# Kernel tuning notes

Measured on AMD Instinct MI355X. Metric: run time of the kernel, lower is better.

Reference implementation:

```python
import jax, jax.numpy as jnp
import numpy as np

B, DIM, HEADS, HH, WW = 4, 256, 8, 48, 48
N = HH * WW
CS = DIM // 4  # channels per crpe split / lowpass split = 64
POOL_SIZES = (1, 2, 3, 6)


def _constrain(kern, k):
    # kern: (C, C, k*k-1); insert the constrained -1 center tap, reshape to OIHW
    C = kern.shape[0]
    ctr = (k * k) // 2
    full = jnp.concatenate(
        [kern[:, :, :ctr], -jnp.ones((C, C, 1), kern.dtype), kern[:, :, ctr:]], axis=2)
    return full.reshape(C, C, k, k)


def _conv(x, w, k):
    p = k // 2
    return jax.lax.conv_general_dilated(
        x, w, (1, 1), [(p, p), (p, p)],
        dimension_numbers=('NCHW', 'OIHW', 'NCHW'))


def _upsample_bilinear_ac(x, H, W):
    # bilinear, align_corners=True, from (B,C,sh,sw) to (B,C,H,W)
    Bc, Cc, sh, sw = x.shape
    if sh == 1 and sw == 1:
        return jnp.broadcast_to(x, (Bc, Cc, H, W))
    ys = jnp.arange(H, dtype=x.dtype) * ((sh - 1) / (H - 1))
    xs = jnp.arange(W, dtype=x.dtype) * ((sw - 1) / (W - 1))
    y0 = jnp.floor(ys).astype(jnp.int32)
    x0 = jnp.floor(xs).astype(jnp.int32)
    y1 = jnp.minimum(y0 + 1, sh - 1)
    x1 = jnp.minimum(x0 + 1, sw - 1)
    wy = (ys - y0.astype(x.dtype))[:, None]
    wx = (xs - x0.astype(x.dtype))[None, :]
    v00 = x[:, :, y0[:, None], x0[None, :]]
    v01 = x[:, :, y0[:, None], x1[None, :]]
    v10 = x[:, :, y1[:, None], x0[None, :]]
    v11 = x[:, :, y1[:, None], x1[None, :]]
    return (v00 * (1 - wy) * (1 - wx) + v01 * (1 - wy) * wx
            + v10 * wy * (1 - wx) + v11 * wy * wx)


def _lowpass(v):
    # v: (B,C,H,W); H,W divisible by all pool sizes -> adaptive pool == uniform block mean
    Bc, Cc, Hc, Wc = v.shape
    outs = []
    for c, s in zip(jnp.split(v, 4, axis=1), POOL_SIZES):
        p = c.reshape(Bc, Cc // 4, s, Hc // s, s, Wc // s).mean(axis=(3, 5))
        outs.append(_upsample_bilinear_ac(p, Hc, Wc))
    return jax.nn.relu(jnp.concatenate(outs, axis=1))


def _crpe(q, res, Hc, Wc, kern3, kern5, kern7):
    # q: (B,h,N,Ch); res: (B,N,C)
    Bc, h, Nc, Ch = q.shape
    C = h * Ch
    v = res.transpose(0, 2, 1).reshape(Bc, C, Hc, Wc)
    lp = _lowpass(v)
    v0, v1, v2, v3 = jnp.split(v, 4, axis=1)
    conv_v = jnp.concatenate([
        v0,
        _conv(v1, _constrain(kern3, 3), 3),
        _conv(v2, _constrain(kern5, 5), 5),
        _conv(v3, _constrain(kern7, 7), 7)], axis=1)
    conv_v = conv_v.reshape(Bc, h, Ch, Nc).transpose(0, 1, 3, 2)  # B h N Ch
    lp = lp.reshape(Bc, h, Ch, Nc).transpose(0, 1, 3, 2)
    return q * conv_v + lp


def setup_inputs() -> dict:
    key = jax.random.key(0)
    ks = jax.random.split(key, 9)
    x = jax.random.normal(ks[0], (B, N, DIM), jnp.float32)
    wq = jax.random.normal(ks[1], (DIM, DIM), jnp.float32) * 0.02
    wkv = jax.random.normal(ks[2], (2 * DIM, DIM), jnp.float32) * 0.02
    wres = jax.random.normal(ks[3], (DIM, DIM), jnp.float32) * 0.02
    wproj = jax.random.normal(ks[4], (DIM, DIM), jnp.float32) * 0.02
    bproj = jnp.zeros((DIM,), jnp.float32)
    def base_kernel(k, kk):
        kern = jax.random.uniform(k, (CS, CS, kk * kk - 1), jnp.float32)
        return kern / kern.sum(axis=2, keepdims=True)
    kern3 = base_kernel(ks[5], 3)
    kern5 = base_kernel(ks[6], 5)
    kern7 = base_kernel(ks[7], 7)
    return {'x': x, 'H': HH, 'W': WW, 'wq': wq, 'wkv': wkv, 'wres': wres,
            'wproj': wproj, 'bproj': bproj, 'kern3': kern3, 'kern5': kern5,
            'kern7': kern7}


def reference(x, H, W, wq, wkv, wres, wproj, bproj, kern3, kern5, kern7):
    Bc, Nc, C = x.shape
    h = HEADS
    Ch = C // h
    scale = Ch ** -0.5
    q = (x @ wq.T).reshape(Bc, Nc, h, Ch).transpose(0, 2, 1, 3)          # B h N Ch
    kv = (x @ wkv.T).reshape(Bc, Nc, 2, h, Ch).transpose(2, 0, 3, 1, 4)  # 2 B h N Ch
    k, v = kv[0], kv[1]
    attn = jax.nn.softmax(jnp.einsum('bhnc,bhmc->bhnm', q * scale, k), axis=-1)
    res = jax.nn.relu(x @ wres.T)
    crpe = _crpe(q, res, H, W, kern3, kern5, kern7)
    out = (jnp.einsum('bhnm,bhmc->bhnc', attn, v) + crpe)
    out = out.transpose(0, 2, 1, 3).reshape(Bc, Nc, C)
    return out @ wproj.T + bproj
```

## Files before the change

### kernel.cpp

```cpp
#include <hip/hip_runtime.h>
#include <math.h>

#define NTOK 2304
#define DIMC 256

typedef __attribute__((ext_vector_type(8))) short short8;
typedef __attribute__((ext_vector_type(4))) float f32x4;

__device__ __forceinline__ unsigned short f2bf(float f) {
  unsigned u = __float_as_uint(f);
  u += 0x7fffu + ((u >> 16) & 1u);
  return (unsigned short)(u >> 16);
}
__device__ __forceinline__ float bf2f(unsigned short h) {
  return __uint_as_float(((unsigned)h) << 16);
}
__device__ __forceinline__ unsigned pack2(float a, float b) {
  return (unsigned)f2bf(a) | ((unsigned)f2bf(b) << 16);
}
__device__ __forceinline__ float fexp2(float x) {
#if __has_builtin(__builtin_amdgcn_exp2f)
  return __builtin_amdgcn_exp2f(x);
#else
  return exp2f(x);
#endif
}
__device__ __forceinline__ void split4(float4 v, uint2& hp, uint2& lp) {
  unsigned short h0 = f2bf(v.x), h1 = f2bf(v.y), h2 = f2bf(v.z), h3 = f2bf(v.w);
  unsigned short l0 = f2bf(v.x - bf2f(h0)), l1 = f2bf(v.y - bf2f(h1));
  unsigned short l2 = f2bf(v.z - bf2f(h2)), l3 = f2bf(v.w - bf2f(h3));
  hp.x = (unsigned)h0 | ((unsigned)h1 << 16);
  hp.y = (unsigned)h2 | ((unsigned)h3 << 16);
  lp.x = (unsigned)l0 | ((unsigned)l1 << 16);
  lp.y = (unsigned)l2 | ((unsigned)l3 << 16);
}

__global__ __launch_bounds__(256) void k_prep_all(
    const float* __restrict__ x, const float* __restrict__ wq,
    const float* __restrict__ wkv, const float* __restrict__ wres,
    const float* __restrict__ wproj, const float* __restrict__ k3,
    const float* __restrict__ k5, const float* __restrict__ k7,
    unsigned short* __restrict__ xhi, unsigned short* __restrict__ xlo,
    unsigned short* __restrict__ Whi, unsigned short* __restrict__ Wlo,
    unsigned short* __restrict__ pwhi, unsigned short* __restrict__ pwlo,
    unsigned short* __restrict__ wT) {
  int bx = blockIdx.x;
  int tid = threadIdx.x;
  if (bx < 2304) {
    int i = bx * 256 + tid;
    uint2 hp, lp;
    split4(((const float4*)x)[i], hp, lp);
    ((uint2*)xhi)[i] = hp;
    ((uint2*)xlo)[i] = lp;
  } else if (bx < 2560) {
    int idx = (bx - 2304) * 256 + tid;
    int row = idx >> 6, q4 = idx & 63;
    const float* src;
    if (row < 256)      src = wq + (size_t)row * 256;
    else if (row < 768) src = wkv + (size_t)(row - 256) * 256;
    else                src = wres + (size_t)(row - 768) * 256;
    uint2 hp, lp;
    split4(*(const float4*)(src + q4 * 4), hp, lp);
    ((uint2*)Whi)[idx] = hp;
    ((uint2*)Wlo)[idx] = lp;
  } else if (bx < 2624) {
    int idx = (bx - 2560) * 256 + tid;
    uint2 hp, lp;
    split4(((const float4*)wproj)[idx], hp, lp);
    ((uint2*)pwhi)[idx] = hp;
    ((uint2*)pwlo)[idx] = lp;
  } else {
    int idx = (bx - 2624) * 256 + tid;
    const float* src; int K, tloc;
    if (idx < 9 * 4096)       { K = 3; src = k3; tloc = idx >> 12; }
    else if (idx < 34 * 4096) { K = 5; src = k5; tloc = (idx - 9 * 4096) >> 12; }
    else                      { K = 7; src = k7; tloc = (idx - 34 * 4096) >> 12; }
    int r = idx & 4095, oc = r >> 6, ic = r & 63;
    int K2 = K * K, ctr = K2 / 2;
    float v = (tloc == ctr) ? -1.f
            : src[((size_t)oc * 64 + ic) * (K2 - 1) + (tloc < ctr ? tloc : tloc - 1)];
    wT[idx] = f2bf(v);
  }
}

__global__ __launch_bounds__(512, 2) void k_gemm_qkvres_mfma(
    const unsigned short* __restrict__ xhi, const unsigned short* __restrict__ xlo,
    const unsigned short* __restrict__ Whi, const unsigned short* __restrict__ Wlo,
    float* __restrict__ qb, unsigned short* __restrict__ khi,
    unsigned short* __restrict__ klo, unsigned short* __restrict__ vT,
    float* __restrict__ resb, unsigned short* __restrict__ resT) {
  __shared__ __align__(16) unsigned short Ah[128 * 64];
  __shared__ __align__(16) unsigned short Al[128 * 64];
  __shared__ __align__(16) unsigned short Bh[128 * 64];
  __shared__ __align__(16) unsigned short Bl[128 * 64];
  const int tid = threadIdx.x;
  const int row0 = blockIdx.x * 128;
  const int col0 = blockIdx.y * 128;
  const int w = tid >> 6, lane = tid & 63, lg = lane >> 4, lc = lane & 15;
  const int wm = w >> 1, wn = w & 1;

  f32x4 acc[2][4];
#pragma unroll
  for (int i = 0; i < 2; ++i)
#pragma unroll
    for (int j = 0; j < 4; ++j) acc[i][j] = (f32x4){0.f, 0.f, 0.f, 0.f};

  for (int kc = 0; kc < 256; kc += 64) {
    __syncthreads();
#pragma unroll
    for (int l = 0; l < 2; ++l) {
      int idx = tid + l * 512;
      int r = idx >> 3, o = idx & 7;
      int sl = ((o ^ (r & 7))) * 8;
      *(uint4*)&Ah[r * 64 + sl] = *(const uint4*)&xhi[(size_t)(row0 + r) * 256 + kc + o * 8];
      *(uint4*)&Al[r * 64 + sl] = *(const uint4*)&xlo[(size_t)(row0 + r) * 256 + kc + o * 8];
      *(uint4*)&Bh[r * 64 + sl] = *(const uint4*)&Whi[(size_t)(col0 + r) * 256 + kc + o * 8];
      *(uint4*)&Bl[r * 64 + sl] = *(const uint4*)&Wlo[(size_t)(col0 + r) * 256 + kc + o * 8];
    }
    __syncthreads();
#pragma unroll
    for (int ks = 0; ks < 2; ++ks) {
      short8 ah[2], al[2], bh[4], bl[4];
#pragma unroll
      for (int mi = 0; mi < 2; ++mi) {
        int r = wm * 32 + mi * 16 + lc;
        int sl = (((ks * 4 + lg) ^ (r & 7))) * 8;
        ah[mi] = *(short8*)&Ah[r * 64 + sl];
        al[mi] = *(short8*)&Al[r * 64 + sl];
      }
#pragma unroll
      for (int ni = 0; ni < 4; ++ni) {
        int r = wn * 64 + ni * 16 + lc;
        int sl = (((ks * 4 + lg) ^ (r & 7))) * 8;
        bh[ni] = *(short8*)&Bh[r * 64 + sl];
        bl[ni] = *(short8*)&Bl[r * 64 + sl];
      }
#pragma unroll
      for (int mi = 0; mi < 2; ++mi)
#pragma unroll
        for (int ni = 0; ni < 4; ++ni) {
          acc[mi][ni] = __builtin_amdgcn_mfma_f32_16x16x32_bf16(ah[mi], bh[ni], acc[mi][ni], 0, 0, 0);
          acc[mi][ni] = __builtin_amdgcn_mfma_f32_16x16x32_bf16(ah[mi], bl[ni], acc[mi][ni], 0, 0, 0);
          acc[mi][ni] = __builtin_amdgcn_mfma_f32_16x16x32_bf16(al[mi], bh[ni], acc[mi][ni], 0, 0, 0);
        }
    }
  }

#pragma unroll
  for (int mi = 0; mi < 2; ++mi) {
    int rbase = row0 + wm * 32 + mi * 16 + lg * 4;
#pragma unroll
    for (int ni = 0; ni < 4; ++ni) {
      int col = col0 + wn * 64 + ni * 16 + lc;
#pragma unroll
      for (int j = 0; j < 4; ++j) {
        int row = rbase + j;
        int b = row / NTOK, n = row % NTOK;
        float vv = acc[mi][ni][j];
        if (col < 256) {
          int head = col >> 5, ch = col & 31;
          qb[(((size_t)b * 8 + head) * NTOK + n) * 32 + ch] = vv;
        } else if (col < 512) {
          int o = col - 256; int head = o >> 5, ch = o & 31;
          size_t idx = (((size_t)b * 8 + head) * NTOK + n) * 32 + ch;
          unsigned short h = f2bf(vv);
          khi[idx] = h;
          klo[idx] = f2bf(vv - bf2f(h));
        } else if (col < 768) {
          int o = col - 512; int head = o >> 5, ch = o & 31;
          vT[(((size_t)b * 8 + head) * 32 + ch) * NTOK + n] = f2bf(vv);
        } else {
          int c = col - 768;
          float rv = fmaxf(vv, 0.f);
          resb[((size_t)b * 256 + c) * NTOK + n] = rv;
          if (c >= 64) {
            int g = (c >> 6) - 1, ic = c & 63;
            resT[(((size_t)b * 3 + g) * NTOK + n) * 64 + ic] = f2bf(rv);
          }
        }
      }
    }
  }
}

__device__ __forceinline__ void softmax_pv(
    f32x4 (&s)[8], float& m_r, float& l_r, f32x4& o0, f32x4& o1,
    int lg, int lc, int srcA, unsigned short (*vs)[136]) {
  float mx[8];
#pragma unroll
  for (int nt = 0; nt < 8; ++nt)
    mx[nt] = fmaxf(fmaxf(s[nt][0], s[nt][1]), fmaxf(s[nt][2], s[nt][3]));
  float mloc = fmaxf(fmaxf(fmaxf(mx[0], mx[1]), fmaxf(mx[2], mx[3])),
                     fmaxf(fmaxf(mx[4], mx[5]), fmaxf(mx[6], mx[7])));

  if (__any(mloc > m_r + 8.f)) {
    float mt = mloc;
    mt = fmaxf(mt, __shfl_xor(mt, 16, 64));
    mt = fmaxf(mt, __shfl_xor(mt, 32, 64));
    float mn = fmaxf(m_r, mt);
    float corr = fexp2(m_r - mn);
    m_r = mn;
    l_r *= corr;
#pragma unroll
    for (int j = 0; j < 4; ++j) {
      float cj = __shfl(corr, lg * 4 + j, 64);
      o0[j] *= cj;
      o1[j] *= cj;
    }
  }

  float ls = 0.f;
#pragma unroll
  for (int nt = 0; nt < 8; ++nt)
#pragma unroll
    for (int j = 0; j < 4; ++j) {
      float p = fexp2(s[nt][j] - m_r);
      s[nt][j] = p;
      ls += p;
    }
  l_r += ls;

  unsigned W[8][2];
#pragma unroll
  for (int nt = 0; nt < 8; ++nt) {
    W[nt][0] = pack2(s[nt][0], s[nt][1]);
    W[nt][1] = pack2(s[nt][2], s[nt][3]);
  }

  __builtin_amdgcn_s_setprio(1);
#pragma unroll
  for (int h2 = 0; h2 < 4; ++h2) {
    unsigned v0 = (lg & 2) ? W[2 * h2 + 1][0] : W[2 * h2][0];
    unsigned v1 = (lg & 2) ? W[2 * h2 + 1][1] : W[2 * h2][1];
    union { unsigned u[4]; short8 v; } pa;
    pa.u[0] = (unsigned)__shfl((int)v0, srcA, 64);
    pa.u[1] = (unsigned)__shfl((int)v1, srcA, 64);
    pa.u[2] = (unsigned)__shfl((int)v0, srcA + 16, 64);
    pa.u[3] = (unsigned)__shfl((int)v1, srcA + 16, 64);
    short8 vf0 = *(short8*)&vs[lc][h2 * 32 + lg * 8];
    short8 vf1 = *(short8*)&vs[lc + 16][h2 * 32 + lg * 8];
    o0 = __builtin_amdgcn_mfma_f32_16x16x32_bf16(pa.v, vf0, o0, 0, 0, 0);
    o1 = __builtin_amdgcn_mfma_f32_16x16x32_bf16(pa.v, vf1, o1, 0, 0, 0);
  }
  __builtin_amdgcn_s_setprio(0);
}

__device__ __forceinline__ void attn_body(
    int bh, int qt, int tid,
    const float* __restrict__ qb, const unsigned short* __restrict__ khi,
    const unsigned short* __restrict__ klo, const unsigned short* __restrict__ vT,
    float* __restrict__ accb,
    unsigned short (*ks_hi)[40], unsigned short (*vs)[136]) {
  const int r0 = qt * 64;
  const int w = tid >> 6;
  const int lane = tid & 63;
  const int lg = lane >> 4;
  const int lc = lane & 15;

  const float scale = 0.17677669529663688f * 1.4426950408889634f;

  const float* qp = qb + (((size_t)bh * NTOK + r0 + w * 16 + lc) * 32 + lg * 8);
  float qf[8];
  *(float4*)&qf[0] = *(const float4*)qp;
  *(float4*)&qf[4] = *(const float4*)(qp + 4);
  short8 qh, ql;
#pragma unroll
  for (int i = 0; i < 8; ++i) {
    float v = qf[i] * scale;
    unsigned short h = f2bf(v);
    qh[i] = (short)h;
    ql[i] = (short)f2bf(v - bf2f(h));
  }

  float m_r = -1.0e30f;
  float l_r = 0.f;
  f32x4 o0 = {0.f, 0.f, 0.f, 0.f};
  f32x4 o1 = {0.f, 0.f, 0.f, 0.f};

  const int krow = tid >> 1, kseg = (tid & 1) * 16;
  const int vrow = tid >> 3, vseg = (tid & 7) * 16;

  const unsigned short* khs = khi + ((size_t)bh * NTOK + krow) * 32 + kseg;
  const unsigned short* vsrc = vT + ((size_t)bh * 32 + vrow) * NTOK + vseg;
  const unsigned short* klp = klo + ((size_t)bh * NTOK + lc) * 32 + lg * 8;

  uint4 ph0 = *(const uint4*)khs,  ph1 = *(const uint4*)(khs + 8);
  uint4 pv0 = *(const uint4*)vsrc, pv1 = *(const uint4*)(vsrc + 8);

  const int srcA = ((lg & 1) * 2) * 16 + lc;

  for (int kt = 0; kt < 18; ++kt) {
    const int kv0 = kt * 128;
    __syncthreads();
    *(uint4*)&ks_hi[krow][kseg]     = ph0;
    *(uint4*)&ks_hi[krow][kseg + 8] = ph1;
    *(uint4*)&vs[vrow][vseg]        = pv0;
    *(uint4*)&vs[vrow][vseg + 8]    = pv1;
    __syncthreads();

    if (kt < 17) {
      size_t ko = (size_t)(kt + 1) * 128 * 32;
      int vo = (kt + 1) * 128;
      ph0 = *(const uint4*)(khs + ko);  ph1 = *(const uint4*)(khs + ko + 8);
      pv0 = *(const uint4*)(vsrc + vo); pv1 = *(const uint4*)(vsrc + vo + 8);
    }

    f32x4 s[8];
#pragma unroll
    for (int half = 0; half < 2; ++half) {
      short8 klr[4];
#pragma unroll
      for (int q = 0; q < 4; ++q)
        klr[q] = *(const short8*)(klp + (size_t)(kv0 + (half * 4 + q) * 16) * 32);
      __builtin_amdgcn_s_setprio(1);
#pragma unroll
      for (int q = 0; q < 4; ++q) {
        int nt = half * 4 + q;
        short8 kh = *(short8*)&ks_hi[nt * 16 + lc][lg * 8];
        f32x4 a = {0.f, 0.f, 0.f, 0.f};
        a = __builtin_amdgcn_mfma_f32_16x16x32_bf16(kh, qh, a, 0, 0, 0);
        a = __builtin_amdgcn_mfma_f32_16x16x32_bf16(klr[q], qh, a, 0, 0, 0);
        a = __builtin_amdgcn_mfma_f32_16x16x32_bf16(kh, ql, a, 0, 0, 0);
        s[nt] = a;
      }
      __builtin_amdgcn_s_setprio(0);
    }

    softmax_pv(s, m_r, l_r, o0, o1, lg, lc, srcA, vs);
  }

  float lfull = l_r;
  lfull += __shfl_xor(lfull, 16, 64);
  lfull += __shfl_xor(lfull, 32, 64);

  float* op = accb + ((size_t)bh * NTOK + r0 + w * 16) * 32;
#pragma unroll
  for (int j = 0; j < 4; ++j) {
    float lj = __shfl(lfull, lg * 4 + j, 64);
    float inv = 1.f / lj;
    int r = lg * 4 + j;
    op[r * 32 + lc] = o0[j] * inv;
    op[r * 32 + lc + 16] = o1[j] * inv;
  }
}

template <int K>
__device__ __forceinline__ void conv_body(
    const unsigned short* __restrict__ plane,
    const unsigned short* __restrict__ wTg,
    float* __restrict__ outg,
    int y, int w, int lane, unsigned short* lds) {
  constexpr int P = K / 2;
  const int tid = w * 64 + lane;
  const int lg = lane >> 4, lc = lane & 15;
  const int oc0 = w * 16;

  uint4 zz = {0, 0, 0, 0};
  for (int i = tid; i < K * 224; i += 256) ((uint4*)lds)[i] = zz;
  __syncthreads();

  f32x4 acc[3];
  acc[0] = acc[1] = acc[2] = (f32x4){0.f, 0.f, 0.f, 0.f};

#pragma unroll
  for (int c = 0; c < 2; ++c) {
    for (int idx = tid; idx < K * 192; idx += 256) {
      int i = idx / 192, rem = idx % 192;
      int gx = rem >> 2, o = rem & 3;
      int gy = y + i - P;
      if ((unsigned)gy < 48u) {
        uint4 v = *(const uint4*)(plane + ((size_t)(gy * 48 + gx)) * 64 + c * 32 + o * 8);
        int slot = gx + P;
        *(uint4*)(lds + ((size_t)i * 56 + slot) * 32 + ((o ^ ((slot >> 1) & 3)) * 8)) = v;
      }
    }
    __syncthreads();

    for (int ky = 0; ky < K; ++ky) {
#pragma unroll
      for (int kx = 0; kx < K; ++kx) {
        const int tap = ky * K + kx;
        short8 aw = *(const short8*)(wTg + (size_t)tap * 4096 + (oc0 + lc) * 64 +
                                     c * 32 + lg * 8);
#pragma unroll
        for (int u = 0; u < 3; ++u) {
          int slot = u * 16 + lc + kx;
          short8 bv = *(short8*)(lds + ((size_t)(ky * 56 + slot)) * 32 +
                                 ((lg ^ ((slot >> 1) & 3)) * 8));
          acc[u] = __builtin_amdgcn_mfma_f32_16x16x32_bf16(aw, bv, acc[u], 0, 0, 0);
        }
      }
    }
    __syncthreads();
  }

#pragma unroll
  for (int u = 0; u < 3; ++u)
#pragma unroll
    for (int j = 0; j < 4; ++j)
      outg[(size_t)(oc0 + lg * 4 + j) * NTOK + y * 48 + u * 16 + lc] = acc[u][j];
}

__device__ __forceinline__ void pool_body(
    const float* __restrict__ resb, float* __restrict__ pooled,
    int task, int lane) {
  const int sArr[4] = {1, 2, 3, 6};
  int g = task >> 8, rem = task & 255;
  int b = rem >> 6, cc = rem & 63;
  int c = g * 64 + cc;
  int S = sArr[g];
  int WSZ = 48 / S, NPX = WSZ * WSZ;
  const float* src = resb + ((size_t)b * 256 + c) * NTOK;
  const float inv = 1.f / NPX;
  for (int w = 0; w < S * S; ++w) {
    int wy = w / S, wx = w % S;
    float sum = 0.f;
    for (int idx = lane; idx < NPX; idx += 64) {
      int yy = wy * WSZ + idx / WSZ;
      int xx = wx * WSZ + idx % WSZ;
      sum += src[yy * 48 + xx];
    }
#pragma unroll
    for (int msk = 1; msk < 64; msk <<= 1) sum += __shfl_xor(sum, msk, 64);
    if (lane == 0) pooled[((size_t)b * 256 + c) * 36 + w] = sum * inv;
  }
}

__global__ __launch_bounds__(256, 4) void k_fat(
    const float* __restrict__ qb, const unsigned short* __restrict__ khi,
    const unsigned short* __restrict__ klo, const unsigned short* __restrict__ vT,
    float* __restrict__ accb, const unsigned short* __restrict__ resT,
    const unsigned short* __restrict__ wT, float* __restrict__ convb,
    const float* __restrict__ resb, float* __restrict__ pooled) {
  __shared__ __align__(16) unsigned char smem[25088];
  const int bx = blockIdx.x;
  const int tid = threadIdx.x;
  if (bx < 1152) {
    unsigned short (*ks_hi)[40] = (unsigned short(*)[40])(smem);
    unsigned short (*vs)[136]   = (unsigned short(*)[136])(smem + 10240);
    attn_body(bx & 31, bx >> 5, tid, qb, khi, klo, vT, accb, ks_hi, vs);
  } else if (bx < 1728) {
    int cid = bx - 1152;
    int g = cid % 3, rest = cid / 3;
    int b = rest / 48, y = rest % 48;
    const unsigned short* plane = resT + (((size_t)b * 3 + g) * NTOK) * 64;
    float* outg = convb + ((size_t)b * 192 + g * 64) * NTOK;
    unsigned short* lds = (unsigned short*)smem;
    int w = tid >> 6, lane = tid & 63;
    if (g == 0)      conv_body<3>(plane, wT,             outg, y, w, lane, lds);
    else if (g == 1) conv_body<5>(plane, wT + 9 * 4096,  outg, y, w, lane, lds);
    else             conv_body<7>(plane, wT + 34 * 4096, outg, y, w, lane, lds);
  } else {
    int task = (bx - 1728) * 4 + (tid >> 6);
    pool_body(resb, pooled, task, tid & 63);
  }
}

__global__ void k_combine(
    const float* __restrict__ qb, const float* __restrict__ accb,
    const float* __restrict__ resb, const float* __restrict__ convb,
    const float* __restrict__ pooled, unsigned short* __restrict__ preh,
    unsigned short* __restrict__ prel) {
  int nt = blockIdx.x;
  int head = blockIdx.y;
  int b = blockIdx.z;
  int tid = threadIdx.x;
  int n = nt * 8 + (tid >> 5);
  int ch = tid & 31;
  int c = head * 32 + ch;
  int g = c >> 6;
  const int sArr[4] = {1, 2, 3, 6};
  int s = sArr[g];

  size_t qidx = (((size_t)b * 8 + head) * NTOK + n) * 32 + ch;
  float qv = qb[qidx];
  float av = accb[qidx];
  float cvv = (g == 0) ? resb[((size_t)b * 256 + c) * NTOK + n]
                       : convb[((size_t)b * 192 + (c - 64)) * NTOK + n];
  const float* pl = pooled + ((size_t)b * 256 + c) * 36;
  float lp;
  if (s == 1) {
    lp = pl[0];
  } else {
    int yy = n / 48, xx = n % 48;
    float fs = (float)(s - 1) / 47.0f;
    float ry = yy * fs, rx = xx * fs;
    int y0 = (int)ry, x0 = (int)rx;
    int y1 = min(y0 + 1, s - 1), x1 = min(x0 + 1, s - 1);
    float wy = ry - (float)y0, wx = rx - (float)x0;
    float v00 = pl[y0 * s + x0], v01 = pl[y0 * s + x1];
    float v10 = pl[y1 * s + x0], v11 = pl[y1 * s + x1];
    lp = v00 * (1 - wy) * (1 - wx) + v01 * (1 - wy) * wx +
         v10 * wy * (1 - wx) + v11 * wy * wx;
  }
  lp = fmaxf(lp, 0.f);
  float val = av + qv * cvv + lp;
  unsigned short h = f2bf(val);
  size_t oidx = ((size_t)b * NTOK + n) * 256 + c;
  preh[oidx] = h;
  prel[oidx] = f2bf(val - bf2f(h));
}

__global__ __launch_bounds__(512, 2) void k_gemm_proj_mfma(
    const unsigned short* __restrict__ preh, const unsigned short* __restrict__ prel,
    const unsigned short* __restrict__ pwhi, const unsigned short* __restrict__ pwlo,
    const float* __restrict__ bproj, float* __restrict__ outp) {
  __shared__ __align__(16) unsigned short Ah[64 * 64];
  __shared__ __align__(16) unsigned short Al[64 * 64];
  __shared__ __align__(16) unsigned short Bh[128 * 64];
  __shared__ __align__(16) unsigned short Bl[128 * 64];
  const int tid = threadIdx.x;
  const int row0 = blockIdx.x * 64;
  const int col0 = blockIdx.y * 128;
  const int w = tid >> 6, lane = tid & 63, lg = lane >> 4, lc = lane & 15;
  const int wm = w >> 2, wn = w & 3;

  f32x4 acc[2][2];
#pragma unroll
  for (int i = 0; i < 2; ++i)
#pragma unroll
    for (int j = 0; j < 2; ++j) acc[i][j] = (f32x4){0.f, 0.f, 0.f, 0.f};

  for (int kc = 0; kc < 256; kc += 64) {
    __syncthreads();
    {
      int r = tid >> 3, o = tid & 7;
      int sl = ((o ^ (r & 7))) * 8;
      *(uint4*)&Ah[r * 64 + sl] = *(const uint4*)&preh[(size_t)(row0 + r) * 256 + kc + o * 8];
      *(uint4*)&Al[r * 64 + sl] = *(const uint4*)&prel[(size_t)(row0 + r) * 256 + kc + o * 8];
    }
#pragma unroll
    for (int l = 0; l < 2; ++l) {
      int idx = tid + l * 512;
      int r = idx >> 3, o = idx & 7;
      int sl = ((o ^ (r & 7))) * 8;
      *(uint4*)&Bh[r * 64 + sl] = *(const uint4*)&pwhi[(size_t)(col0 + r) * 256 + kc + o * 8];
      *(uint4*)&Bl[r * 64 + sl] = *(const uint4*)&pwlo[(size_t)(col0 + r) * 256 + kc + o * 8];
    }
    __syncthreads();
#pragma unroll
    for (int ks = 0; ks < 2; ++ks) {
      short8 ah[2], al[2], bh[2], bl[2];
#pragma unroll
      for (int mi = 0; mi < 2; ++mi) {
        int r = wm * 32 + mi * 16 + lc;
        int sl = (((ks * 4 + lg) ^ (r & 7))) * 8;
        ah[mi] = *(short8*)&Ah[r * 64 + sl];
        al[mi] = *(short8*)&Al[r * 64 + sl];
      }
#pragma unroll
      for (int ni = 0; ni < 2; ++ni) {
        int r = wn * 32 + ni * 16 + lc;
        int sl = (((ks * 4 + lg) ^ (r & 7))) * 8;
        bh[ni] = *(short8*)&Bh[r * 64 + sl];
        bl[ni] = *(short8*)&Bl[r * 64 + sl];
      }
#pragma unroll
      for (int mi = 0; mi < 2; ++mi)
#pragma unroll
        for (int ni = 0; ni < 2; ++ni) {
          acc[mi][ni] = __builtin_amdgcn_mfma_f32_16x16x32_bf16(ah[mi], bh[ni], acc[mi][ni], 0, 0, 0);
          acc[mi][ni] = __builtin_amdgcn_mfma_f32_16x16x32_bf16(ah[mi], bl[ni], acc[mi][ni], 0, 0, 0);
          acc[mi][ni] = __builtin_amdgcn_mfma_f32_16x16x32_bf16(al[mi], bh[ni], acc[mi][ni], 0, 0, 0);
        }
    }
  }

#pragma unroll
  for (int mi = 0; mi < 2; ++mi) {
    int rbase = row0 + wm * 32 + mi * 16 + lg * 4;
#pragma unroll
    for (int ni = 0; ni < 2; ++ni) {
      int col = col0 + wn * 32 + ni * 16 + lc;
#pragma unroll
      for (int j = 0; j < 4; ++j)
        outp[(size_t)(rbase + j) * 256 + col] = acc[mi][ni][j] + bproj[col];
    }
  }
}

extern "C" void kernel_launch(void* const* d_in, const int* in_sizes, int n_in,
                              void* d_out, int out_size, void* d_ws, size_t ws_size,
                              hipStream_t stream) {
  const float* x     = (const float*)d_in[0];
  const float* wq    = (const float*)d_in[3];
  const float* wkv   = (const float*)d_in[4];
  const float* wres  = (const float*)d_in[5];
  const float* wproj = (const float*)d_in[6];
  const float* bproj = (const float*)d_in[7];
  const float* kern3 = (const float*)d_in[8];
  const float* kern5 = (const float*)d_in[9];
  const float* kern7 = (const float*)d_in[10];

  const size_t SZ = (size_t)4 * 8 * NTOK * 32;
  float* wsf  = (float*)d_ws;
  float* qb   = wsf;
  float* resb = wsf + SZ;
  float* accb = wsf + 2 * SZ;
  unsigned short* xhi = (unsigned short*)(wsf + 2 * SZ);
  unsigned short* xlo = (unsigned short*)(wsf + 2 * SZ + SZ / 2);
  unsigned short* khi = (unsigned short*)(wsf + 3 * SZ);
  unsigned short* klo = (unsigned short*)(wsf + 3 * SZ + SZ / 2);
  unsigned short* vT  = (unsigned short*)(wsf + 4 * SZ);
  unsigned short* resT = (unsigned short*)(wsf + 4 * SZ + SZ / 2);
  unsigned short* wT   = (unsigned short*)(wsf + 4 * SZ + SZ / 2 + 884736);
  unsigned short* Whi = (unsigned short*)(wsf + 4 * SZ + SZ / 2 + 884736 + 169984);
  unsigned short* Wlo = Whi + 262144;
  unsigned short* preh = (unsigned short*)(wsf + 4 * SZ + SZ / 2);
  unsigned short* prel = (unsigned short*)(wsf + 5 * SZ);
  float* convb  = wsf + SZ * 11 / 2;
  float* pooled = convb + 1769472;
  unsigned short* pwhi = (unsigned short*)(pooled + 36864);
  unsigned short* pwlo = pwhi + 65536;
  float* outp = (float*)d_out;

  k_prep_all<<<dim3(3952), 256, 0, stream>>>(x, wq, wkv, wres, wproj, kern3,
                                             kern5, kern7, xhi, xlo, Whi, Wlo,
                                             pwhi, pwlo, wT);
  k_gemm_qkvres_mfma<<<dim3(72, 8), 512, 0, stream>>>(xhi, xlo, Whi, Wlo, qb, khi,
                                                      klo, vT, resb, resT);
  k_fat<<<dim3(1984), 256, 0, stream>>>(qb, khi, klo, vT, accb, resT, wT, convb,
                                        resb, pooled);
  k_combine<<<dim3(288, 8, 4), 256, 0, stream>>>(qb, accb, resb, convb, pooled,
                                                 preh, prel);
  k_gemm_proj_mfma<<<dim3(144, 2), 512, 0, stream>>>(preh, prel, pwhi, pwlo, bproj, outp);
}
```

Baseline: 169.3 us.

## Load K-hi fragments from global directly and double-buffer V tile in LDS

The attention loop no longer stages the high-precision K tile through shared memory. Each lane now reads its K-hi MFMA fragments straight from global memory, the same way K-lo was already read. The V tile is double-buffered in LDS, so each iteration needs one barrier instead of two, and the store of the next V tile overlaps the current QK MFMAs. The cost is more global load traffic per wave for K, with less reuse across the four waves, plus more register pressure from holding the khr fragments.

After: 189.4 us. 11.9% more time.

```diff
diff --git a/kernel.cpp b/kernel.cpp
--- a/kernel.cpp
+++ b/kernel.cpp
@@ -249,8 +249,7 @@
     int bh, int qt, int tid,
     const float* __restrict__ qb, const unsigned short* __restrict__ khi,
     const unsigned short* __restrict__ klo, const unsigned short* __restrict__ vT,
-    float* __restrict__ accb,
-    unsigned short (*ks_hi)[40], unsigned short (*vs)[136]) {
+    float* __restrict__ accb, unsigned short* vsmem) {
   const int r0 = qt * 64;
   const int w = tid >> 6;
   const int lane = tid & 63;
@@ -277,56 +276,65 @@
   f32x4 o0 = {0.f, 0.f, 0.f, 0.f};
   f32x4 o1 = {0.f, 0.f, 0.f, 0.f};
 
-  const int krow = tid >> 1, kseg = (tid & 1) * 16;
+  unsigned short (*vs0)[136] = (unsigned short(*)[136])vsmem;
+  unsigned short (*vs1)[136] = (unsigned short(*)[136])(vsmem + 32 * 136);
+
   const int vrow = tid >> 3, vseg = (tid & 7) * 16;
-
-  const unsigned short* khs = khi + ((size_t)bh * NTOK + krow) * 32 + kseg;
   const unsigned short* vsrc = vT + ((size_t)bh * 32 + vrow) * NTOK + vseg;
+  const unsigned short* khp = khi + ((size_t)bh * NTOK + lc) * 32 + lg * 8;
   const unsigned short* klp = klo + ((size_t)bh * NTOK + lc) * 32 + lg * 8;
 
-  uint4 ph0 = *(const uint4*)khs,  ph1 = *(const uint4*)(khs + 8);
-  uint4 pv0 = *(const uint4*)vsrc, pv1 = *(const uint4*)(vsrc + 8);
-
   const int srcA = ((lg & 1) * 2) * 16 + lc;
+
+  {
+    uint4 a = *(const uint4*)vsrc;
+    uint4 b = *(const uint4*)(vsrc + 8);
+    *(uint4*)&vs0[vrow][vseg] = a;
+    *(uint4*)&vs0[vrow][vseg + 8] = b;
+  }
+  __syncthreads();
 
   for (int kt = 0; kt < 18; ++kt) {
     const int kv0 = kt * 128;
+    unsigned short (*vcur)[136] = (kt & 1) ? vs1 : vs0;
+    unsigned short (*vnxt)[136] = (kt & 1) ? vs0 : vs1;
+
+    uint4 nv0, nv1;
+    if (kt < 17) {
+      int vo = (kt + 1) * 128;
+      nv0 = *(const uint4*)(vsrc + vo);
+      nv1 = *(const uint4*)(vsrc + vo + 8);
+    }
+
+    f32x4 s[8];
+#pragma unroll
+    for (int half = 0; half < 2; ++half) {
+      short8 khr[4], klr[4];
+#pragma unroll
+      for (int q = 0; q < 4; ++q) {
+        size_t off = (size_t)(kv0 + (half * 4 + q) * 16) * 32;
+        khr[q] = *(const short8*)(khp + off);
+        klr[q] = *(const short8*)(klp + off);
+      }
+      __builtin_amdgcn_s_setprio(1);
+#pragma unroll
+      for (int q = 0; q < 4; ++q) {
+        f32x4 a = {0.f, 0.f, 0.f, 0.f};
+        a = __builtin_amdgcn_mfma_f32_16x16x32_bf16(khr[q], qh, a, 0, 0, 0);
+        a = __builtin_amdgcn_mfma_f32_16x16x32_bf16(klr[q], qh, a, 0, 0, 0);
+        a = __builtin_amdgcn_mfma_f32_16x16x32_bf16(khr[q], ql, a, 0, 0, 0);
+        s[half * 4 + q] = a;
+      }
+      __builtin_amdgcn_s_setprio(0);
+    }
+
+    if (kt < 17) {
+      *(uint4*)&vnxt[vrow][vseg] = nv0;
+      *(uint4*)&vnxt[vrow][vseg + 8] = nv1;
+    }
+
+    softmax_pv(s, m_r, l_r, o0, o1, lg, lc, srcA, vcur);
     __syncthreads();
-    *(uint4*)&ks_hi[krow][kseg]     = ph0;
-    *(uint4*)&ks_hi[krow][kseg + 8] = ph1;
-    *(uint4*)&vs[vrow][vseg]        = pv0;
-    *(uint4*)&vs[vrow][vseg + 8]    = pv1;
-    __syncthreads();
-
-    if (kt < 17) {
-      size_t ko = (size_t)(kt + 1) * 128 * 32;
-      int vo = (kt + 1) * 128;
-      ph0 = *(const uint4*)(khs + ko);  ph1 = *(const uint4*)(khs + ko + 8);
-      pv0 = *(const uint4*)(vsrc + vo); pv1 = *(const uint4*)(vsrc + vo + 8);
-    }
-
-    f32x4 s[8];
-#pragma unroll
-    for (int half = 0; half < 2; ++half) {
-      short8 klr[4];
-#pragma unroll
-      for (int q = 0; q < 4; ++q)
-        klr[q] = *(const short8*)(klp + (size_t)(kv0 + (half * 4 + q) * 16) * 32);
-      __builtin_amdgcn_s_setprio(1);
-#pragma unroll
-      for (int q = 0; q < 4; ++q) {
-        int nt = half * 4 + q;
-        short8 kh = *(short8*)&ks_hi[nt * 16 + lc][lg * 8];
-        f32x4 a = {0.f, 0.f, 0.f, 0.f};
-        a = __builtin_amdgcn_mfma_f32_16x16x32_bf16(kh, qh, a, 0, 0, 0);
-        a = __builtin_amdgcn_mfma_f32_16x16x32_bf16(klr[q], qh, a, 0, 0, 0);
-        a = __builtin_amdgcn_mfma_f32_16x16x32_bf16(kh, ql, a, 0, 0, 0);
-        s[nt] = a;
-      }
-      __builtin_amdgcn_s_setprio(0);
-    }
-
-    softmax_pv(s, m_r, l_r, o0, o1, lg, lc, srcA, vs);
   }
 
   float lfull = l_r;
@@ -436,9 +444,8 @@
   const int bx = blockIdx.x;
   const int tid = threadIdx.x;
   if (bx < 1152) {
-    unsigned short (*ks_hi)[40] = (unsigned short(*)[40])(smem);
-    unsigned short (*vs)[136]   = (unsigned short(*)[136])(smem + 10240);
-    attn_body(bx & 31, bx >> 5, tid, qb, khi, klo, vT, accb, ks_hi, vs);
+    attn_body(bx & 31, bx >> 5, tid, qb, khi, klo, vT, accb,
+              (unsigned short*)smem);
   } else if (bx < 1728) {
     int cid = bx - 1152;
     int g = cid % 3, rest = cid / 3;
```
